# Performance work log

Hardware: AMD Instinct MI355X
Metric: run time of the kernel (lower is better)

## Reference

```python
import jax, jax.numpy as jnp
import numpy as np

DIM = 1024
HEADS = 16
SCALE = DIM ** -0.5  # NOTE: original scales by full dim, not head dim


def setup_inputs() -> dict:
    key = jax.random.key(0)
    ks = jax.random.split(key, 6)
    B, S, D = 2, 2048, DIM
    x = jax.random.normal(ks[0], (B, S, D), dtype=jnp.float32)
    Wq = jax.random.normal(ks[1], (D, D), dtype=jnp.float32) * 0.02
    Wk = jax.random.normal(ks[2], (D, D), dtype=jnp.float32) * 0.02
    Wv = jax.random.normal(ks[3], (D, D), dtype=jnp.float32) * 0.02
    Wo = jax.random.normal(ks[4], (D, D), dtype=jnp.float32) * 0.02
    z = jnp.zeros((D,), dtype=jnp.float32)
    return {"x": x, "Wq": Wq, "bq": z, "Wk": Wk, "bk": z, "Wv": Wv, "bv": z, "Wo": Wo, "bo": z}


def reference(x, Wq, bq, Wk, bk, Wv, bv, Wo, bo):
    B, S, D = x.shape
    H = HEADS
    d = D // H
    # projections (Linear: x @ W + b)
    q = (x @ Wq + bq).reshape(B, S, H, d).transpose(0, 2, 1, 3)  # b h i d
    k = (x @ Wk + bk).reshape(B, S, H, d).transpose(0, 2, 1, 3)  # b h j d
    v = (x @ Wv + bv).reshape(B, S, H, d).transpose(0, 2, 1, 3)  # b h j d
    dots = jnp.einsum("bhid,bhjd->bhij", q, k) * SCALE
    # causal mask: strict upper triangle -> -inf
    mask = jnp.triu(jnp.ones((S, S), dtype=bool), k=1)
    dots = jnp.where(mask, -jnp.inf, dots)
    attn = jax.nn.softmax(dots, axis=-1)
    out = jnp.einsum("bhij,bhjd->bhid", attn, v)
    out = out.transpose(0, 2, 1, 3).reshape(B, S, D)  # b i (h d)
    return out @ Wo + bo
```

## Files before the change

kernel.cpp:

```cpp
#include <hip/hip_runtime.h>
#include <hip/hip_bf16.h>

typedef __bf16 bf16;
typedef __bf16 bf16x4 __attribute__((ext_vector_type(4)));
typedef __bf16 bf16x8 __attribute__((ext_vector_type(8)));
typedef float floatx4 __attribute__((ext_vector_type(4)));

#define MFMA_16x16x32(a, b, c) __builtin_amdgcn_mfma_f32_16x16x32_bf16((a), (b), (c), 0, 0, 0)
#define NEG_INF (-__builtin_inff())

#define CB 2
#define CS 2048
#define CD 1024
#define CH 16
#define CM (CB * CS)
#define QSC (0.03125f * 1.44269504088896340736f)

__device__ __forceinline__ void async16(const bf16* g, bf16* l) {
    __builtin_amdgcn_global_load_lds(
        (const __attribute__((address_space(1))) void*)g,
        (__attribute__((address_space(3))) void*)l, 16, 0, 0);
}

__global__ __launch_bounds__(256) void conv_x(const float* __restrict__ x,
                                              bf16* __restrict__ xb) {
    size_t i = ((size_t)blockIdx.x * 256 + threadIdx.x) * 8;
    float4 a = *(const float4*)(x + i);
    float4 b = *(const float4*)(x + i + 4);
    bf16x8 v;
    v[0] = (bf16)a.x; v[1] = (bf16)a.y; v[2] = (bf16)a.z; v[3] = (bf16)a.w;
    v[4] = (bf16)b.x; v[5] = (bf16)b.y; v[6] = (bf16)b.z; v[7] = (bf16)b.w;
    *(bf16x8*)(xb + i) = v;
}

__global__ __launch_bounds__(256) void conv_wt(
    const float* __restrict__ W0, const float* __restrict__ W1,
    const float* __restrict__ W2, const float* __restrict__ W3,
    bf16* __restrict__ Wt) {
    __shared__ bf16 Ws[64 * 68];
    const float* W = blockIdx.z == 0 ? W0 : blockIdx.z == 1 ? W1
                   : blockIdx.z == 2 ? W2 : W3;
    bf16* out = Wt + (size_t)blockIdx.z * CD * CD;
    const int t = threadIdx.x;
    const int n0 = blockIdx.x * 64, k0 = blockIdx.y * 64;
    const int rr = t >> 4, c4 = (t & 15) * 4;
#pragma unroll
    for (int i = 0; i < 4; i++) {
        int r = rr + i * 16;
        float4 f = *(const float4*)(W + (size_t)(k0 + r) * CD + n0 + c4);
        bf16x4 v;
        v[0] = (bf16)f.x; v[1] = (bf16)f.y; v[2] = (bf16)f.z; v[3] = (bf16)f.w;
        *(bf16x4*)&Ws[r * 68 + c4] = v;
    }
    __syncthreads();
#pragma unroll
    for (int i = 0; i < 4; i++) {
        int n = rr + i * 16;
        bf16x4 v;
#pragma unroll
        for (int j = 0; j < 4; j++) v[j] = Ws[(c4 + j) * 68 + n];
        *(bf16x4*)(out + (size_t)(n0 + n) * CD + k0 + c4) = v;
    }
}

__global__ __launch_bounds__(256) void gemm_qkv(
    const bf16* __restrict__ A, const bf16* __restrict__ Bt,
    const float* __restrict__ bq, const float* __restrict__ bk,
    const float* __restrict__ bv,
    bf16* __restrict__ Qb, bf16* __restrict__ Kb, bf16* __restrict__ Vb) {
    __shared__ bf16 As[128 * 32];
    __shared__ bf16 Bs[128 * 32];
    const int t = threadIdx.x, w = t >> 6, lane = t & 63;
    const int quad = lane >> 4, l15 = lane & 15;
    const int which = blockIdx.x >> 3;
    const int bn = (blockIdx.x & 7) * 128, bm = blockIdx.y * 128;
    const bf16* Bw = Bt + (size_t)which * CD * CD;

    const bf16* ag = A + (size_t)(bm + w * 16 + (lane >> 2)) * CD + (lane & 3) * 8;
    const bf16* bg = Bw + (size_t)(bn + w * 16 + (lane >> 2)) * CD + (lane & 3) * 8;
    const int lo = w * 16 * 32;

    const int wm = (w >> 1) * 64, wn = (w & 1) * 64;
    floatx4 acc[4][4] = {};

    for (int k0 = 0; k0 < CD; k0 += 32) {
        async16(ag + k0, &As[lo]);
        async16(ag + (size_t)64 * CD + k0, &As[lo + 64 * 32]);
        async16(bg + k0, &Bs[lo]);
        async16(bg + (size_t)64 * CD + k0, &Bs[lo + 64 * 32]);
        __syncthreads();
        bf16x8 af[4], bfr[4];
#pragma unroll
        for (int mt = 0; mt < 4; mt++)
            af[mt] = *(const bf16x8*)&As[(wm + mt * 16 + l15) * 32 + quad * 8];
#pragma unroll
        for (int nt = 0; nt < 4; nt++)
            bfr[nt] = *(const bf16x8*)&Bs[(wn + nt * 16 + l15) * 32 + quad * 8];
#pragma unroll
        for (int mt = 0; mt < 4; mt++)
#pragma unroll
            for (int nt = 0; nt < 4; nt++)
                acc[mt][nt] = MFMA_16x16x32(af[mt], bfr[nt], acc[mt][nt]);
        __syncthreads();
    }

    const float* bias = which == 0 ? bq : which == 1 ? bk : bv;
    bf16* out = which == 0 ? Qb : Kb;
#pragma unroll
    for (int mt = 0; mt < 4; mt++) {
#pragma unroll
        for (int nt = 0; nt < 4; nt++) {
            int token = bm + wm + mt * 16 + quad * 4;
            int col = bn + wn + nt * 16 + l15;
            int b = token >> 11, s = token & (CS - 1);
            int h = col >> 6, dd = col & 63;
            if (which == 2) {
                bf16x4 pv;
#pragma unroll
                for (int r = 0; r < 4; r++) pv[r] = (bf16)(acc[mt][nt][r] + bias[col]);
                *(bf16x4*)&Vb[(((size_t)(b * CH + h)) * 64 + dd) * CS + s] = pv;
            } else {
#pragma unroll
                for (int r = 0; r < 4; r++) {
                    float v = acc[mt][nt][r] + bias[col];
                    if (which == 0) v *= QSC;
                    out[(((size_t)(b * CH + h)) * CS + s + r) * 64 + dd] = (bf16)v;
                }
            }
        }
    }
}

__global__ __launch_bounds__(256) void gemm_o(
    const bf16* __restrict__ A, const bf16* __restrict__ Bt,
    const float* __restrict__ bias, float* __restrict__ out) {
    __shared__ bf16 As[64 * 32];
    __shared__ bf16 Bs[128 * 32];
    const int t = threadIdx.x, w = t >> 6, lane = t & 63;
    const int quad = lane >> 4, l15 = lane & 15;
    const int bn = blockIdx.x * 128, bm = blockIdx.y * 64;

    const bf16* ag = A + (size_t)(bm + w * 16 + (lane >> 2)) * CD + (lane & 3) * 8;
    const bf16* bg = Bt + (size_t)(bn + w * 16 + (lane >> 2)) * CD + (lane & 3) * 8;
    const int lo = w * 16 * 32;

    const int wm = (w >> 1) * 32, wn = (w & 1) * 64;
    floatx4 acc[2][4] = {};

    for (int k0 = 0; k0 < CD; k0 += 32) {
        async16(ag + k0, &As[lo]);
        async16(bg + k0, &Bs[lo]);
        async16(bg + (size_t)64 * CD + k0, &Bs[lo + 64 * 32]);
        __syncthreads();
        bf16x8 af[2], bfr[4];
#pragma unroll
        for (int mt = 0; mt < 2; mt++)
            af[mt] = *(const bf16x8*)&As[(wm + mt * 16 + l15) * 32 + quad * 8];
#pragma unroll
        for (int nt = 0; nt < 4; nt++)
            bfr[nt] = *(const bf16x8*)&Bs[(wn + nt * 16 + l15) * 32 + quad * 8];
#pragma unroll
        for (int mt = 0; mt < 2; mt++)
#pragma unroll
            for (int nt = 0; nt < 4; nt++)
                acc[mt][nt] = MFMA_16x16x32(af[mt], bfr[nt], acc[mt][nt]);
        __syncthreads();
    }

#pragma unroll
    for (int mt = 0; mt < 2; mt++)
#pragma unroll
        for (int nt = 0; nt < 4; nt++)
#pragma unroll
            for (int r = 0; r < 4; r++) {
                int row = bm + wm + mt * 16 + quad * 4 + r;
                int col = bn + wn + nt * 16 + l15;
                out[(size_t)row * CD + col] = acc[mt][nt][r] + bias[col];
            }
}

__global__ __launch_bounds__(256) void attn_kernel(
    const bf16* __restrict__ Q, const bf16* __restrict__ Kg,
    const bf16* __restrict__ Vg, bf16* __restrict__ Ob) {
    __shared__ bf16 Ks[64 * 72];
    __shared__ bf16 Vt[64 * 72];
    __shared__ bf16 Pt[4][32 * 72];

    const int t = threadIdx.x;
    const int w = t >> 6, lane = t & 63;
    const int quad = lane >> 4, l15 = lane & 15;

    const int half = blockIdx.x >> 8;
    const int slot = blockIdx.x & 255;
    const int bh   = slot & 31;
    const int qq   = slot >> 5;
    const int qb   = half ? qq : (15 - qq);
    const int q0   = qb * 128;
    const int wrow0 = q0 + w * 32;
    const int nT = 2 * qb + 2;

    const bf16* Qh = Q + (size_t)bh * CS * 64;
    const bf16* Kh = Kg + (size_t)bh * CS * 64;
    const bf16* Vh = Vg + (size_t)bh * 64 * CS;

    const int strow = t >> 2, soff = (t & 3) * 16;
    const bf16* ksrc = Kh + (size_t)strow * 64 + soff;
    const bf16* vsrc = Vh + (size_t)strow * CS + soff;

    bf16x8 kr0 = *(const bf16x8*)ksrc;
    bf16x8 kr1 = *(const bf16x8*)(ksrc + 8);
    bf16x8 vr0 = *(const bf16x8*)vsrc;
    bf16x8 vr1 = *(const bf16x8*)(vsrc + 8);

    bf16x8 qf[2][2];
#pragma unroll
    for (int g = 0; g < 2; g++) {
        const bf16* qsrc = Qh + (size_t)(wrow0 + g * 16 + l15) * 64 + quad * 8;
        qf[g][0] = *(const bf16x8*)qsrc;
        qf[g][1] = *(const bf16x8*)(qsrc + 32);
    }

    floatx4 o[4][2] = {};
    float m_r[2] = {NEG_INF, NEG_INF}, l_r[2] = {0.f, 0.f};

    bf16* pw = Pt[w];

    for (int kt = 0; kt < nT; kt++) {
        const int ks0 = kt * 64;
        __syncthreads();
        *(bf16x8*)&Ks[strow * 72 + soff]     = kr0;
        *(bf16x8*)&Ks[strow * 72 + soff + 8] = kr1;
        *(bf16x8*)&Vt[strow * 72 + soff]     = vr0;
        *(bf16x8*)&Vt[strow * 72 + soff + 8] = vr1;
        __syncthreads();
        {
            int nk = (kt + 1 < nT) ? kt + 1 : 0;
            const bf16* kn = ksrc + (size_t)nk * 64 * 64;
            const bf16* vn = vsrc + nk * 64;
            kr0 = *(const bf16x8*)kn;
            kr1 = *(const bf16x8*)(kn + 8);
            vr0 = *(const bf16x8*)vn;
            vr1 = *(const bf16x8*)(vn + 8);
        }
        if (ks0 > wrow0 + 31) continue;

        floatx4 sc[2][4] = {};
#pragma unroll
        for (int nt = 0; nt < 4; nt++) {
            bf16x8 af0 = *(const bf16x8*)&Ks[(nt * 16 + l15) * 72 + quad * 8];
            bf16x8 af1 = *(const bf16x8*)&Ks[(nt * 16 + l15) * 72 + 32 + quad * 8];
#pragma unroll
            for (int g = 0; g < 2; g++) {
                sc[g][nt] = MFMA_16x16x32(af0, qf[g][0], sc[g][nt]);
                sc[g][nt] = MFMA_16x16x32(af1, qf[g][1], sc[g][nt]);
            }
        }
        if (ks0 + 63 > wrow0) {
#pragma unroll
            for (int g = 0; g < 2; g++) {
                int qrow = wrow0 + g * 16 + l15;
#pragma unroll
                for (int nt = 0; nt < 4; nt++)
#pragma unroll
                    for (int r = 0; r < 4; r++)
                        if (ks0 + nt * 16 + quad * 4 + r > qrow)
                            sc[g][nt][r] = NEG_INF;
            }
        }
        float alpha_g[2];
#pragma unroll
        for (int g = 0; g < 2; g++) {
            float mx = NEG_INF;
#pragma unroll
            for (int nt = 0; nt < 4; nt++)
#pragma unroll
                for (int r = 0; r < 4; r++) mx = fmaxf(mx, sc[g][nt][r]);
            mx = fmaxf(mx, __shfl_xor(mx, 16));
            mx = fmaxf(mx, __shfl_xor(mx, 32));
            float mn = fmaxf(m_r[g], mx);
            alpha_g[g] = __builtin_amdgcn_exp2f(m_r[g] - mn);
            m_r[g] = mn;
            float sum = 0.f;
#pragma unroll
            for (int nt = 0; nt < 4; nt++)
#pragma unroll
                for (int r = 0; r < 4; r++) {
                    sc[g][nt][r] = __builtin_amdgcn_exp2f(sc[g][nt][r] - mn);
                    sum += sc[g][nt][r];
                }
            sum += __shfl_xor(sum, 16);
            sum += __shfl_xor(sum, 32);
            l_r[g] = l_r[g] * alpha_g[g] + sum;
        }
#pragma unroll
        for (int g = 0; g < 2; g++)
#pragma unroll
            for (int nt = 0; nt < 4; nt++) {
                bf16x4 pk;
#pragma unroll
                for (int r = 0; r < 4; r++) pk[r] = (bf16)sc[g][nt][r];
                *(bf16x4*)&pw[(g * 16 + l15) * 72 + nt * 16 + quad * 4] = pk;
            }
        bf16x8 bp[2][2];
#pragma unroll
        for (int g = 0; g < 2; g++) {
            bp[g][0] = *(const bf16x8*)&pw[(g * 16 + l15) * 72 + quad * 8];
            bp[g][1] = *(const bf16x8*)&pw[(g * 16 + l15) * 72 + 32 + quad * 8];
        }
#pragma unroll
        for (int dt = 0; dt < 4; dt++)
#pragma unroll
            for (int g = 0; g < 2; g++)
#pragma unroll
                for (int r = 0; r < 4; r++) o[dt][g][r] *= alpha_g[g];
#pragma unroll
        for (int dt = 0; dt < 4; dt++) {
            bf16x8 av0 = *(const bf16x8*)&Vt[(dt * 16 + l15) * 72 + quad * 8];
            bf16x8 av1 = *(const bf16x8*)&Vt[(dt * 16 + l15) * 72 + 32 + quad * 8];
#pragma unroll
            for (int g = 0; g < 2; g++) {
                o[dt][g] = MFMA_16x16x32(av0, bp[g][0], o[dt][g]);
                o[dt][g] = MFMA_16x16x32(av1, bp[g][1], o[dt][g]);
            }
        }
    }

    const int b = bh >> 4, h = bh & 15;
#pragma unroll
    for (int g = 0; g < 2; g++) {
        float rl = 1.f / l_r[g];
        int row = wrow0 + g * 16 + l15;
#pragma unroll
        for (int dt = 0; dt < 4; dt++) {
            bf16x4 ov;
#pragma unroll
            for (int r = 0; r < 4; r++) ov[r] = (bf16)(o[dt][g][r] * rl);
            *(bf16x4*)&Ob[((size_t)b * CS + row) * CD + h * 64 + dt * 16 + quad * 4] = ov;
        }
    }
}

extern "C" void kernel_launch(void* const* d_in, const int* in_sizes, int n_in,
                              void* d_out, int out_size, void* d_ws, size_t ws_size,
                              hipStream_t stream) {
    const float* x  = (const float*)d_in[0];
    const float* Wq = (const float*)d_in[1];
    const float* bq = (const float*)d_in[2];
    const float* Wk = (const float*)d_in[3];
    const float* bk = (const float*)d_in[4];
    const float* Wv = (const float*)d_in[5];
    const float* bv = (const float*)d_in[6];
    const float* Wo = (const float*)d_in[7];
    const float* bo = (const float*)d_in[8];
    float* out = (float*)d_out;

    bf16* xb = (bf16*)d_ws;
    bf16* Wt = xb + (size_t)CM * CD;
    bf16* Qb = Wt + (size_t)4 * CD * CD;
    bf16* Kb = Qb + (size_t)CB * CH * CS * 64;
    bf16* Vb = Kb + (size_t)CB * CH * CS * 64;
    bf16* Ob = Vb + (size_t)CB * CH * CS * 64;

    conv_x<<<(CM * CD) / (256 * 8), 256, 0, stream>>>(x, xb);
    conv_wt<<<dim3(CD / 64, CD / 64, 4), 256, 0, stream>>>(Wq, Wk, Wv, Wo, Wt);

    gemm_qkv<<<dim3(24, CM / 128), 256, 0, stream>>>(
        xb, Wt, bq, bk, bv, Qb, Kb, Vb);

    attn_kernel<<<512, 256, 0, stream>>>(Qb, Kb, Vb, Ob);

    gemm_o<<<dim3(8, CM / 64), 256, 0, stream>>>(
        Ob, Wt + (size_t)3 * CD * CD, bo, out);
}
```

Measured before the change: 193.2 us.

## Double-buffer K/V tiles in LDS and lazily rescale the online softmax

The attention kernel now keeps two LDS buffers for K and V. The next tile is written into the idle buffer while the current one is consumed, which drops one block-wide barrier per iteration. The online softmax only rescales the accumulators and running sum when some row's maximum grows by more than 8 (log2 units). The per-row sum reduction across lanes moves out of the loop to the final normalization. MFMA sections are wrapped in s_setprio hints. The costs are doubled K/V LDS use, which may lower occupancy, and unnormalized exponentials that can reach up to 2^8.

```diff
diff --git a/kernel.cpp b/kernel.cpp
--- a/kernel.cpp
+++ b/kernel.cpp
@@ -182,8 +182,8 @@
 __global__ __launch_bounds__(256) void attn_kernel(
     const bf16* __restrict__ Q, const bf16* __restrict__ Kg,
     const bf16* __restrict__ Vg, bf16* __restrict__ Ob) {
-    __shared__ bf16 Ks[64 * 72];
-    __shared__ bf16 Vt[64 * 72];
+    __shared__ bf16 Ks[2][64 * 72];
+    __shared__ bf16 Vt[2][64 * 72];
     __shared__ bf16 Pt[4][32 * 72];
 
     const int t = threadIdx.x;
@@ -206,11 +206,20 @@
     const int strow = t >> 2, soff = (t & 3) * 16;
     const bf16* ksrc = Kh + (size_t)strow * 64 + soff;
     const bf16* vsrc = Vh + (size_t)strow * CS + soff;
+    const int sbase = strow * 72 + soff;
 
     bf16x8 kr0 = *(const bf16x8*)ksrc;
     bf16x8 kr1 = *(const bf16x8*)(ksrc + 8);
     bf16x8 vr0 = *(const bf16x8*)vsrc;
     bf16x8 vr1 = *(const bf16x8*)(vsrc + 8);
+    *(bf16x8*)&Ks[0][sbase]     = kr0;
+    *(bf16x8*)&Ks[0][sbase + 8] = kr1;
+    *(bf16x8*)&Vt[0][sbase]     = vr0;
+    *(bf16x8*)&Vt[0][sbase + 8] = vr1;
+    kr0 = *(const bf16x8*)(ksrc + 64 * 64);
+    kr1 = *(const bf16x8*)(ksrc + 64 * 64 + 8);
+    vr0 = *(const bf16x8*)(vsrc + 64);
+    vr1 = *(const bf16x8*)(vsrc + 64 + 8);
 
     bf16x8 qf[2][2];
 #pragma unroll
@@ -221,20 +230,22 @@
     }
 
     floatx4 o[4][2] = {};
-    float m_r[2] = {NEG_INF, NEG_INF}, l_r[2] = {0.f, 0.f};
+    float m_r[2] = {NEG_INF, NEG_INF};
+    float l_r[2] = {0.f, 0.f};
 
     bf16* pw = Pt[w];
 
     for (int kt = 0; kt < nT; kt++) {
+        const int cur = kt & 1;
         const int ks0 = kt * 64;
         __syncthreads();
-        *(bf16x8*)&Ks[strow * 72 + soff]     = kr0;
-        *(bf16x8*)&Ks[strow * 72 + soff + 8] = kr1;
-        *(bf16x8*)&Vt[strow * 72 + soff]     = vr0;
-        *(bf16x8*)&Vt[strow * 72 + soff + 8] = vr1;
-        __syncthreads();
+
+        *(bf16x8*)&Ks[cur ^ 1][sbase]     = kr0;
+        *(bf16x8*)&Ks[cur ^ 1][sbase + 8] = kr1;
+        *(bf16x8*)&Vt[cur ^ 1][sbase]     = vr0;
+        *(bf16x8*)&Vt[cur ^ 1][sbase + 8] = vr1;
         {
-            int nk = (kt + 1 < nT) ? kt + 1 : 0;
+            int nk = (kt + 2 < nT) ? kt + 2 : 0;
             const bf16* kn = ksrc + (size_t)nk * 64 * 64;
             const bf16* vn = vsrc + nk * 64;
             kr0 = *(const bf16x8*)kn;
@@ -244,17 +255,22 @@
         }
         if (ks0 > wrow0 + 31) continue;
 
+        const bf16* ksb = Ks[cur];
+        const bf16* vtb = Vt[cur];
+
         floatx4 sc[2][4] = {};
+        __builtin_amdgcn_s_setprio(1);
 #pragma unroll
         for (int nt = 0; nt < 4; nt++) {
-            bf16x8 af0 = *(const bf16x8*)&Ks[(nt * 16 + l15) * 72 + quad * 8];
-            bf16x8 af1 = *(const bf16x8*)&Ks[(nt * 16 + l15) * 72 + 32 + quad * 8];
+            bf16x8 af0 = *(const bf16x8*)&ksb[(nt * 16 + l15) * 72 + quad * 8];
+            bf16x8 af1 = *(const bf16x8*)&ksb[(nt * 16 + l15) * 72 + 32 + quad * 8];
 #pragma unroll
             for (int g = 0; g < 2; g++) {
                 sc[g][nt] = MFMA_16x16x32(af0, qf[g][0], sc[g][nt]);
                 sc[g][nt] = MFMA_16x16x32(af1, qf[g][1], sc[g][nt]);
             }
         }
+        __builtin_amdgcn_s_setprio(0);
         if (ks0 + 63 > wrow0) {
 #pragma unroll
             for (int g = 0; g < 2; g++) {
@@ -267,30 +283,43 @@
                             sc[g][nt][r] = NEG_INF;
             }
         }
-        float alpha_g[2];
+        float mx[2];
 #pragma unroll
         for (int g = 0; g < 2; g++) {
-            float mx = NEG_INF;
+            float m = NEG_INF;
 #pragma unroll
             for (int nt = 0; nt < 4; nt++)
 #pragma unroll
-                for (int r = 0; r < 4; r++) mx = fmaxf(mx, sc[g][nt][r]);
-            mx = fmaxf(mx, __shfl_xor(mx, 16));
-            mx = fmaxf(mx, __shfl_xor(mx, 32));
-            float mn = fmaxf(m_r[g], mx);
-            alpha_g[g] = __builtin_amdgcn_exp2f(m_r[g] - mn);
-            m_r[g] = mn;
-            float sum = 0.f;
+                for (int r = 0; r < 4; r++) m = fmaxf(m, sc[g][nt][r]);
+            m = fmaxf(m, __shfl_xor(m, 16));
+            m = fmaxf(m, __shfl_xor(m, 32));
+            mx[g] = m;
+        }
+        int need = (mx[0] > m_r[0] + 8.f) || (mx[1] > m_r[1] + 8.f);
+        if (__any(need)) {
+#pragma unroll
+            for (int g = 0; g < 2; g++) {
+                float mn = fmaxf(m_r[g], mx[g]);
+                float a = __builtin_amdgcn_exp2f(m_r[g] - mn);
+                m_r[g] = mn;
+                l_r[g] *= a;
+#pragma unroll
+                for (int dt = 0; dt < 4; dt++)
+#pragma unroll
+                    for (int r = 0; r < 4; r++) o[dt][g][r] *= a;
+            }
+        }
+#pragma unroll
+        for (int g = 0; g < 2; g++) {
+            float s = 0.f;
 #pragma unroll
             for (int nt = 0; nt < 4; nt++)
 #pragma unroll
                 for (int r = 0; r < 4; r++) {
-                    sc[g][nt][r] = __builtin_amdgcn_exp2f(sc[g][nt][r] - mn);
-                    sum += sc[g][nt][r];
+                    sc[g][nt][r] = __builtin_amdgcn_exp2f(sc[g][nt][r] - m_r[g]);
+                    s += sc[g][nt][r];
                 }
-            sum += __shfl_xor(sum, 16);
-            sum += __shfl_xor(sum, 32);
-            l_r[g] = l_r[g] * alpha_g[g] + sum;
+            l_r[g] += s;
         }
 #pragma unroll
         for (int g = 0; g < 2; g++)
@@ -307,28 +336,27 @@
             bp[g][0] = *(const bf16x8*)&pw[(g * 16 + l15) * 72 + quad * 8];
             bp[g][1] = *(const bf16x8*)&pw[(g * 16 + l15) * 72 + 32 + quad * 8];
         }
-#pragma unroll
-        for (int dt = 0; dt < 4; dt++)
-#pragma unroll
-            for (int g = 0; g < 2; g++)
-#pragma unroll
-                for (int r = 0; r < 4; r++) o[dt][g][r] *= alpha_g[g];
+        __builtin_amdgcn_s_setprio(1);
 #pragma unroll
         for (int dt = 0; dt < 4; dt++) {
-            bf16x8 av0 = *(const bf16x8*)&Vt[(dt * 16 + l15) * 72 + quad * 8];
-            bf16x8 av1 = *(const bf16x8*)&Vt[(dt * 16 + l15) * 72 + 32 + quad * 8];
+            bf16x8 av0 = *(const bf16x8*)&vtb[(dt * 16 + l15) * 72 + quad * 8];
+            bf16x8 av1 = *(const bf16x8*)&vtb[(dt * 16 + l15) * 72 + 32 + quad * 8];
 #pragma unroll
             for (int g = 0; g < 2; g++) {
                 o[dt][g] = MFMA_16x16x32(av0, bp[g][0], o[dt][g]);
                 o[dt][g] = MFMA_16x16x32(av1, bp[g][1], o[dt][g]);
             }
         }
+        __builtin_amdgcn_s_setprio(0);
     }
 
     const int b = bh >> 4, h = bh & 15;
 #pragma unroll
     for (int g = 0; g < 2; g++) {
-        float rl = 1.f / l_r[g];
+        float l = l_r[g];
+        l += __shfl_xor(l, 16);
+        l += __shfl_xor(l, 32);
+        float rl = 1.f / l;
         int row = wrow0 + g * 16 + l15;
 #pragma unroll
         for (int dt = 0; dt < 4; dt++) {
```

New measurement: 191.7 us. No clear change (-0.8%).
